# Kernel optimization log

Measured on AMD Instinct MI355X. Metric: run time of the kernel, lower is better.

The kernel has to match this reference:

```python
import jax, jax.numpy as jnp
import numpy as np

NUM_USERS = 100000
NUM_ITEMS = 100000
EMBED_DIM = 64
BATCH = 4096
MAX_NEIGH = 50


def setup_inputs() -> dict:
    key = jax.random.key(0)
    ks = jax.random.split(key, 12)
    d = EMBED_DIM
    nodes = jax.random.randint(ks[0], (BATCH,), 0, NUM_USERS)
    neighbors = jax.random.randint(ks[1], (BATCH, MAX_NEIGH), 0, NUM_ITEMS)
    lengths = 1 + jax.random.randint(ks[2], (BATCH,), 0, MAX_NEIGH)  # ragged sizes in [1, MAX_NEIGH]
    u_table = jax.random.normal(ks[3], (NUM_USERS, d), dtype=jnp.float32) * 0.1
    i_table = jax.random.normal(ks[4], (NUM_ITEMS, d), dtype=jnp.float32) * 0.1
    # GraphRec-style attention MLP: Linear(2d,d) -> relu -> Linear(d,d) -> relu -> Linear(d,1) -> softmax
    W1 = jax.random.normal(ks[5], (2 * d, d), dtype=jnp.float32) * (1.0 / np.sqrt(2 * d))
    b1 = jnp.zeros((d,), dtype=jnp.float32)
    W2 = jax.random.normal(ks[6], (d, d), dtype=jnp.float32) * (1.0 / np.sqrt(d))
    b2 = jnp.zeros((d,), dtype=jnp.float32)
    W3 = jax.random.normal(ks[7], (d, 1), dtype=jnp.float32) * (1.0 / np.sqrt(d))
    b3 = jnp.zeros((1,), dtype=jnp.float32)
    return {"u_table": u_table, "i_table": i_table, "W1": W1, "b1": b1,
            "W2": W2, "b2": b2, "W3": W3, "b3": b3,
            "nodes": nodes, "neighbors": neighbors, "lengths": lengths}


def reference(u_table, i_table, W1, b1, W2, b2, W3, b3, nodes, neighbors, lengths):
    # is_user=True: gather item features for neighbors, user feature for the node itself.
    neighs = i_table[neighbors]            # [B, L, d]
    node = u_table[nodes]                  # [B, d]
    B, L, d = neighs.shape
    x = jnp.concatenate([neighs, jnp.broadcast_to(node[:, None, :], (B, L, d))], axis=-1)  # [B, L, 2d]
    h = jax.nn.relu(x @ W1 + b1)           # [B, L, d]
    h = jax.nn.relu(h @ W2 + b2)           # [B, L, d]
    logits = (h @ W3 + b3)[..., 0]         # [B, L]
    mask = jnp.arange(L)[None, :] < lengths[:, None]  # ragged neighbor mask
    logits = jnp.where(mask, logits, -jnp.inf)
    att = jax.nn.softmax(logits, axis=1)   # softmax over each node's neighbors (dim=0 per-node in torch)
    # embedding = (neighs^T att)^T  ==  sum_l att[b,l] * neighs[b,l,:]
    return jnp.einsum("bl,bld->bd", att, neighs)  # [B, d]
```

## Files before the change

### kernel.cpp

```cpp
#include <hip/hip_runtime.h>
#include <math.h>

#define LMAX  50
#define NWAVE 2048

typedef short bf16x8 __attribute__((ext_vector_type(8)));
typedef float f32x4  __attribute__((ext_vector_type(4)));
union bfu { bf16x8 v; unsigned u[4]; };

__device__ __forceinline__ unsigned cvt_pk(float lo, float hi) {
    unsigned r;
    asm("v_cvt_pk_bf16_f32 %0, %1, %2" : "=v"(r) : "v"(lo), "v"(hi));
    return r;
}
__device__ __forceinline__ bf16x8 cvt8f(float4 a, float4 b) {
    bfu r;
    r.u[0] = cvt_pk(a.x, a.y); r.u[1] = cvt_pk(a.z, a.w);
    r.u[2] = cvt_pk(b.x, b.y); r.u[3] = cvt_pk(b.z, b.w);
    return r.v;
}

__device__ __forceinline__ void process_elem(
    const float* __restrict__ i_table, float* __restrict__ out,
    int b, int len, const int (&idx)[6],
    bf16x8 axu0, bf16x8 axu1,
    const bf16x8 (&w1f)[4][4], const bf16x8 (&w2f)[2][4],
    const float (&b1v)[4], const float (&b2v)[4], const float (&w3v)[4],
    unsigned short* __restrict__ hw, float* __restrict__ Lsw,
    int l15, int g)
{
    const int g8    = g * 8;
    const int ntile = (len + 15) >> 4;

    float4 LA[2][4];
    #define ISSUE_T(t) if ((t) < ntile) { \
        const float* xp = i_table + (size_t)idx[t] * 64 + g8; \
        LA[(t) & 1][0] = *(const float4*)(xp); \
        LA[(t) & 1][1] = *(const float4*)(xp + 4); \
        LA[(t) & 1][2] = *(const float4*)(xp + 32); \
        LA[(t) & 1][3] = *(const float4*)(xp + 36); \
    }
    ISSUE_T(0)
    ISSUE_T(1)

    f32x4 hn[4];
    #pragma unroll
    for (int nt = 0; nt < 4; ++nt)
        hn[nt] = (f32x4){b1v[nt], b1v[nt], b1v[nt], b1v[nt]};
    #pragma unroll
    for (int nt = 0; nt < 4; ++nt)
        hn[nt] = __builtin_amdgcn_mfma_f32_16x16x32_bf16(axu0, w1f[2][nt], hn[nt], 0, 0, 0);
    #pragma unroll
    for (int nt = 0; nt < 4; ++nt)
        hn[nt] = __builtin_amdgcn_mfma_f32_16x16x32_bf16(axu1, w1f[3][nt], hn[nt], 0, 0, 0);

    float m = -INFINITY, ssum = 0.f;
    float accW[16];
    #pragma unroll
    for (int i = 0; i < 16; ++i) accW[i] = 0.f;

    #pragma unroll
    for (int t = 0; t < 4; ++t) {
        if (t < ntile) {
            bf16x8 a0 = cvt8f(LA[t & 1][0], LA[t & 1][1]);
            bf16x8 a1 = cvt8f(LA[t & 1][2], LA[t & 1][3]);
            if (t + 2 < 4) ISSUE_T(t + 2)

            f32x4 acc[4];
            #pragma unroll
            for (int nt = 0; nt < 4; ++nt) acc[nt] = hn[nt];
            #pragma unroll
            for (int nt = 0; nt < 4; ++nt)
                acc[nt] = __builtin_amdgcn_mfma_f32_16x16x32_bf16(a0, w1f[0][nt], acc[nt], 0, 0, 0);
            #pragma unroll
            for (int nt = 0; nt < 4; ++nt)
                acc[nt] = __builtin_amdgcn_mfma_f32_16x16x32_bf16(a1, w1f[1][nt], acc[nt], 0, 0, 0);

            #pragma unroll
            for (int nt = 0; nt < 4; ++nt) {
                unsigned p0 = cvt_pk(fmaxf(acc[nt][0], 0.f), fmaxf(acc[nt][1], 0.f));
                unsigned p1 = cvt_pk(fmaxf(acc[nt][2], 0.f), fmaxf(acc[nt][3], 0.f));
                hw[(g * 4 + 0) * 72 + nt * 16 + l15] = (unsigned short)p0;
                hw[(g * 4 + 1) * 72 + nt * 16 + l15] = (unsigned short)(p0 >> 16);
                hw[(g * 4 + 2) * 72 + nt * 16 + l15] = (unsigned short)p1;
                hw[(g * 4 + 3) * 72 + nt * 16 + l15] = (unsigned short)(p1 >> 16);
            }
            bf16x8 h0 = *(const bf16x8*)&hw[l15 * 72 + g8];
            bf16x8 h1 = *(const bf16x8*)&hw[l15 * 72 + 32 + g8];

            f32x4 c2[4];
            #pragma unroll
            for (int nt = 0; nt < 4; ++nt)
                c2[nt] = (f32x4){b2v[nt], b2v[nt], b2v[nt], b2v[nt]};
            #pragma unroll
            for (int nt = 0; nt < 4; ++nt)
                c2[nt] = __builtin_amdgcn_mfma_f32_16x16x32_bf16(h0, w2f[0][nt], c2[nt], 0, 0, 0);
            #pragma unroll
            for (int nt = 0; nt < 4; ++nt)
                c2[nt] = __builtin_amdgcn_mfma_f32_16x16x32_bf16(h1, w2f[1][nt], c2[nt], 0, 0, 0);

            float sv[4];
            #pragma unroll
            for (int reg = 0; reg < 4; ++reg) {
                float s = 0.f;
                #pragma unroll
                for (int nt = 0; nt < 4; ++nt)
                    s = fmaf(fmaxf(c2[nt][reg], 0.f), w3v[nt], s);
                s += __shfl_xor(s, 1); s += __shfl_xor(s, 2);
                s += __shfl_xor(s, 4); s += __shfl_xor(s, 8);
                if (t * 16 + g * 4 + reg >= len) s = -INFINITY;
                sv[reg] = s;
            }

            float tm = fmaxf(fmaxf(sv[0], sv[1]), fmaxf(sv[2], sv[3]));
            tm = fmaxf(tm, __shfl_xor(tm, 16));
            tm = fmaxf(tm, __shfl_xor(tm, 32));
            if (tm > m) {
                const float nm = tm;
                const float sc = __expf(m - nm);
                ssum *= sc;
                #pragma unroll
                for (int i = 0; i < 16; ++i) accW[i] *= sc;
                m = nm;
            }
            float e0 = __expf(sv[0] - m), e1 = __expf(sv[1] - m);
            float e2 = __expf(sv[2] - m), e3 = __expf(sv[3] - m);
            float es = (e0 + e1) + (e2 + e3);
            es += __shfl_xor(es, 16);
            es += __shfl_xor(es, 32);
            ssum += es;

            if (l15 == 0) *(float4*)&Lsw[g * 4] = make_float4(e0, e1, e2, e3);
            const float er = Lsw[l15];

            #pragma unroll
            for (int i = 0; i < 8; ++i) {
                union { unsigned u; float f; } lo, hi2;
                lo.u  = ((unsigned)(unsigned short)a0[i]) << 16;
                hi2.u = ((unsigned)(unsigned short)a1[i]) << 16;
                accW[i]     = fmaf(er, lo.f,  accW[i]);
                accW[8 + i] = fmaf(er, hi2.f, accW[8 + i]);
            }
        }
    }
    #undef ISSUE_T

    #pragma unroll
    for (int i = 0; i < 16; ++i) {
        accW[i] += __shfl_xor(accW[i], 1);
        accW[i] += __shfl_xor(accW[i], 2);
        accW[i] += __shfl_xor(accW[i], 4);
        accW[i] += __shfl_xor(accW[i], 8);
    }
    const float inv = 1.f / ssum;
    if (l15 == 0) {
        float4 o0 = make_float4(accW[0] * inv,  accW[1] * inv,  accW[2] * inv,  accW[3] * inv);
        float4 o1 = make_float4(accW[4] * inv,  accW[5] * inv,  accW[6] * inv,  accW[7] * inv);
        float4 o2 = make_float4(accW[8] * inv,  accW[9] * inv,  accW[10] * inv, accW[11] * inv);
        float4 o3 = make_float4(accW[12] * inv, accW[13] * inv, accW[14] * inv, accW[15] * inv);
        *(float4*)(out + b * 64 +      g8)     = o0;
        *(float4*)(out + b * 64 +      g8 + 4) = o1;
        *(float4*)(out + b * 64 + 32 + g8)     = o2;
        *(float4*)(out + b * 64 + 32 + g8 + 4) = o3;
    }
}

__global__ __launch_bounds__(256, 2) void graphrec_k(
    const float* __restrict__ u_table, const float* __restrict__ i_table,
    const float* __restrict__ W1, const float* __restrict__ b1,
    const float* __restrict__ W2, const float* __restrict__ b2,
    const float* __restrict__ W3, const float* __restrict__ b3,
    const int* __restrict__ nodes, const int* __restrict__ neighbors,
    const int* __restrict__ lengths, float* __restrict__ out)
{
    __shared__ __attribute__((aligned(16))) short WL[24][64][8];
    __shared__ __attribute__((aligned(16))) unsigned short Hs[4][16 * 72];
    __shared__ float Ls[4][16];

    const int tid  = threadIdx.x;
    const int w    = tid >> 6, lane = tid & 63;
    const int l15  = lane & 15, g = lane >> 4, g8 = g * 8;

    for (int f = w; f < 24; f += 4) {
        const float* Ws = (f < 16) ? W1 : W2;
        const int    fi = (f < 16) ? f : f - 16;
        const int    ks = fi >> 2, nt = fi & 3;
        const float* p  = Ws + (ks * 32 + g8) * 64 + nt * 16 + l15;
        bfu r;
        r.u[0] = cvt_pk(p[0 * 64], p[1 * 64]);
        r.u[1] = cvt_pk(p[2 * 64], p[3 * 64]);
        r.u[2] = cvt_pk(p[4 * 64], p[5 * 64]);
        r.u[3] = cvt_pk(p[6 * 64], p[7 * 64]);
        *(bf16x8*)&WL[f][lane][0] = r.v;
    }
    __syncthreads();

    bf16x8 w1f[4][4], w2f[2][4];
    #pragma unroll
    for (int ks = 0; ks < 4; ++ks)
        #pragma unroll
        for (int nt = 0; nt < 4; ++nt)
            w1f[ks][nt] = *(const bf16x8*)&WL[ks * 4 + nt][lane][0];
    #pragma unroll
    for (int ks = 0; ks < 2; ++ks)
        #pragma unroll
        for (int nt = 0; nt < 4; ++nt)
            w2f[ks][nt] = *(const bf16x8*)&WL[16 + ks * 4 + nt][lane][0];

    float b1v[4], b2v[4], w3v[4];
    #pragma unroll
    for (int nt = 0; nt < 4; ++nt) {
        b1v[nt] = b1[nt * 16 + l15];
        b2v[nt] = b2[nt * 16 + l15];
        w3v[nt] = W3[nt * 16 + l15];
    }

    const int wid = blockIdx.x * 4 + w;
    const int b0  = wid, b1e = wid + NWAVE;

    const int len0 = lengths[b0], len1 = lengths[b1e];
    const int nd0  = nodes[b0],   nd1  = nodes[b1e];

    int idx0[6] = {0, 0, 0, 0, 0, 0}, idx1[6] = {0, 0, 0, 0, 0, 0};
    const int nt0 = (len0 + 15) >> 4, nt1 = (len1 + 15) >> 4;
    #pragma unroll
    for (int t = 0; t < 4; ++t) {
        int r = t * 16 + l15; if (r >= len0) r = len0 - 1;
        if (t < nt0) idx0[t] = neighbors[b0 * LMAX + r];
    }
    #pragma unroll
    for (int t = 0; t < 4; ++t) {
        int r = t * 16 + l15; if (r >= len1) r = len1 - 1;
        if (t < nt1) idx1[t] = neighbors[b1e * LMAX + r];
    }

    const float* up0 = u_table + (size_t)nd0 * 64 + g8;
    const float* up1 = u_table + (size_t)nd1 * 64 + g8;
    float4 U00 = *(const float4*)(up0);
    float4 U01 = *(const float4*)(up0 + 4);
    float4 U02 = *(const float4*)(up0 + 32);
    float4 U03 = *(const float4*)(up0 + 36);
    float4 U10 = *(const float4*)(up1);
    float4 U11 = *(const float4*)(up1 + 4);
    float4 U12 = *(const float4*)(up1 + 32);
    float4 U13 = *(const float4*)(up1 + 36);

    process_elem(i_table, out, b0, len0, idx0,
                 cvt8f(U00, U01), cvt8f(U02, U03),
                 w1f, w2f, b1v, b2v, w3v, &Hs[w][0], &Ls[w][0], l15, g);

    process_elem(i_table, out, b1e, len1, idx1,
                 cvt8f(U10, U11), cvt8f(U12, U13),
                 w1f, w2f, b1v, b2v, w3v, &Hs[w][0], &Ls[w][0], l15, g);
}

extern "C" void kernel_launch(void* const* d_in, const int* in_sizes, int n_in,
                              void* d_out, int out_size, void* d_ws, size_t ws_size,
                              hipStream_t stream) {
    const float* u_table   = (const float*)d_in[0];
    const float* i_table   = (const float*)d_in[1];
    const float* W1        = (const float*)d_in[2];
    const float* b1        = (const float*)d_in[3];
    const float* W2        = (const float*)d_in[4];
    const float* b2        = (const float*)d_in[5];
    const float* W3        = (const float*)d_in[6];
    const float* b3        = (const float*)d_in[7];
    const int*   nodes     = (const int*)d_in[8];
    const int*   neighbors = (const int*)d_in[9];
    const int*   lengths   = (const int*)d_in[10];
    float* out = (float*)d_out;

    graphrec_k<<<dim3(NWAVE / 4), dim3(256), 0, stream>>>(
        u_table, i_table, W1, b1, W2, b2, W3, b3, nodes, neighbors, lengths, out);
}
```

Measured before the change: 22.83 us.

## Process one batch element per wave and issue all gathers before weight staging

Each wave now handles a single batch element instead of two, which doubles the grid to 1024 blocks. All neighbor-row gathers (up to four tiles) and the user-row load are issued up front, before the weights are converted into shared memory, so gather latency overlaps with the weight setup and the barrier. The node-side W1 fragments are read directly from LDS rather than kept in registers, which frees registers for the larger in-flight load buffer. In exchange, every block repeats the weight conversion for half as many elements, and the indices past the row length fall back to lane 0's index via readlane.

```diff
diff --git a/kernel.cpp b/kernel.cpp
--- a/kernel.cpp
+++ b/kernel.cpp
@@ -1,8 +1,8 @@
 #include <hip/hip_runtime.h>
 #include <math.h>
 
-#define LMAX  50
-#define NWAVE 2048
+#define LMAX 50
+#define NB   4096
 
 typedef short bf16x8 __attribute__((ext_vector_type(8)));
 typedef float f32x4  __attribute__((ext_vector_type(4)));
@@ -19,150 +19,9 @@
     r.u[2] = cvt_pk(b.x, b.y); r.u[3] = cvt_pk(b.z, b.w);
     return r.v;
 }
-
-__device__ __forceinline__ void process_elem(
-    const float* __restrict__ i_table, float* __restrict__ out,
-    int b, int len, const int (&idx)[6],
-    bf16x8 axu0, bf16x8 axu1,
-    const bf16x8 (&w1f)[4][4], const bf16x8 (&w2f)[2][4],
-    const float (&b1v)[4], const float (&b2v)[4], const float (&w3v)[4],
-    unsigned short* __restrict__ hw, float* __restrict__ Lsw,
-    int l15, int g)
-{
-    const int g8    = g * 8;
-    const int ntile = (len + 15) >> 4;
-
-    float4 LA[2][4];
-    #define ISSUE_T(t) if ((t) < ntile) { \
-        const float* xp = i_table + (size_t)idx[t] * 64 + g8; \
-        LA[(t) & 1][0] = *(const float4*)(xp); \
-        LA[(t) & 1][1] = *(const float4*)(xp + 4); \
-        LA[(t) & 1][2] = *(const float4*)(xp + 32); \
-        LA[(t) & 1][3] = *(const float4*)(xp + 36); \
-    }
-    ISSUE_T(0)
-    ISSUE_T(1)
-
-    f32x4 hn[4];
-    #pragma unroll
-    for (int nt = 0; nt < 4; ++nt)
-        hn[nt] = (f32x4){b1v[nt], b1v[nt], b1v[nt], b1v[nt]};
-    #pragma unroll
-    for (int nt = 0; nt < 4; ++nt)
-        hn[nt] = __builtin_amdgcn_mfma_f32_16x16x32_bf16(axu0, w1f[2][nt], hn[nt], 0, 0, 0);
-    #pragma unroll
-    for (int nt = 0; nt < 4; ++nt)
-        hn[nt] = __builtin_amdgcn_mfma_f32_16x16x32_bf16(axu1, w1f[3][nt], hn[nt], 0, 0, 0);
-
-    float m = -INFINITY, ssum = 0.f;
-    float accW[16];
-    #pragma unroll
-    for (int i = 0; i < 16; ++i) accW[i] = 0.f;
-
-    #pragma unroll
-    for (int t = 0; t < 4; ++t) {
-        if (t < ntile) {
-            bf16x8 a0 = cvt8f(LA[t & 1][0], LA[t & 1][1]);
-            bf16x8 a1 = cvt8f(LA[t & 1][2], LA[t & 1][3]);
-            if (t + 2 < 4) ISSUE_T(t + 2)
-
-            f32x4 acc[4];
-            #pragma unroll
-            for (int nt = 0; nt < 4; ++nt) acc[nt] = hn[nt];
-            #pragma unroll
-            for (int nt = 0; nt < 4; ++nt)
-                acc[nt] = __builtin_amdgcn_mfma_f32_16x16x32_bf16(a0, w1f[0][nt], acc[nt], 0, 0, 0);
-            #pragma unroll
-            for (int nt = 0; nt < 4; ++nt)
-                acc[nt] = __builtin_amdgcn_mfma_f32_16x16x32_bf16(a1, w1f[1][nt], acc[nt], 0, 0, 0);
-
-            #pragma unroll
-            for (int nt = 0; nt < 4; ++nt) {
-                unsigned p0 = cvt_pk(fmaxf(acc[nt][0], 0.f), fmaxf(acc[nt][1], 0.f));
-                unsigned p1 = cvt_pk(fmaxf(acc[nt][2], 0.f), fmaxf(acc[nt][3], 0.f));
-                hw[(g * 4 + 0) * 72 + nt * 16 + l15] = (unsigned short)p0;
-                hw[(g * 4 + 1) * 72 + nt * 16 + l15] = (unsigned short)(p0 >> 16);
-                hw[(g * 4 + 2) * 72 + nt * 16 + l15] = (unsigned short)p1;
-                hw[(g * 4 + 3) * 72 + nt * 16 + l15] = (unsigned short)(p1 >> 16);
-            }
-            bf16x8 h0 = *(const bf16x8*)&hw[l15 * 72 + g8];
-            bf16x8 h1 = *(const bf16x8*)&hw[l15 * 72 + 32 + g8];
-
-            f32x4 c2[4];
-            #pragma unroll
-            for (int nt = 0; nt < 4; ++nt)
-                c2[nt] = (f32x4){b2v[nt], b2v[nt], b2v[nt], b2v[nt]};
-            #pragma unroll
-            for (int nt = 0; nt < 4; ++nt)
-                c2[nt] = __builtin_amdgcn_mfma_f32_16x16x32_bf16(h0, w2f[0][nt], c2[nt], 0, 0, 0);
-            #pragma unroll
-            for (int nt = 0; nt < 4; ++nt)
-                c2[nt] = __builtin_amdgcn_mfma_f32_16x16x32_bf16(h1, w2f[1][nt], c2[nt], 0, 0, 0);
-
-            float sv[4];
-            #pragma unroll
-            for (int reg = 0; reg < 4; ++reg) {
-                float s = 0.f;
-                #pragma unroll
-                for (int nt = 0; nt < 4; ++nt)
-                    s = fmaf(fmaxf(c2[nt][reg], 0.f), w3v[nt], s);
-                s += __shfl_xor(s, 1); s += __shfl_xor(s, 2);
-                s += __shfl_xor(s, 4); s += __shfl_xor(s, 8);
-                if (t * 16 + g * 4 + reg >= len) s = -INFINITY;
-                sv[reg] = s;
-            }
-
-            float tm = fmaxf(fmaxf(sv[0], sv[1]), fmaxf(sv[2], sv[3]));
-            tm = fmaxf(tm, __shfl_xor(tm, 16));
-            tm = fmaxf(tm, __shfl_xor(tm, 32));
-            if (tm > m) {
-                const float nm = tm;
-                const float sc = __expf(m - nm);
-                ssum *= sc;
-                #pragma unroll
-                for (int i = 0; i < 16; ++i) accW[i] *= sc;
-                m = nm;
-            }
-            float e0 = __expf(sv[0] - m), e1 = __expf(sv[1] - m);
-            float e2 = __expf(sv[2] - m), e3 = __expf(sv[3] - m);
-            float es = (e0 + e1) + (e2 + e3);
-            es += __shfl_xor(es, 16);
-            es += __shfl_xor(es, 32);
-            ssum += es;
-
-            if (l15 == 0) *(float4*)&Lsw[g * 4] = make_float4(e0, e1, e2, e3);
-            const float er = Lsw[l15];
-
-            #pragma unroll
-            for (int i = 0; i < 8; ++i) {
-                union { unsigned u; float f; } lo, hi2;
-                lo.u  = ((unsigned)(unsigned short)a0[i]) << 16;
-                hi2.u = ((unsigned)(unsigned short)a1[i]) << 16;
-                accW[i]     = fmaf(er, lo.f,  accW[i]);
-                accW[8 + i] = fmaf(er, hi2.f, accW[8 + i]);
-            }
-        }
-    }
-    #undef ISSUE_T
-
-    #pragma unroll
-    for (int i = 0; i < 16; ++i) {
-        accW[i] += __shfl_xor(accW[i], 1);
-        accW[i] += __shfl_xor(accW[i], 2);
-        accW[i] += __shfl_xor(accW[i], 4);
-        accW[i] += __shfl_xor(accW[i], 8);
-    }
-    const float inv = 1.f / ssum;
-    if (l15 == 0) {
-        float4 o0 = make_float4(accW[0] * inv,  accW[1] * inv,  accW[2] * inv,  accW[3] * inv);
-        float4 o1 = make_float4(accW[4] * inv,  accW[5] * inv,  accW[6] * inv,  accW[7] * inv);
-        float4 o2 = make_float4(accW[8] * inv,  accW[9] * inv,  accW[10] * inv, accW[11] * inv);
-        float4 o3 = make_float4(accW[12] * inv, accW[13] * inv, accW[14] * inv, accW[15] * inv);
-        *(float4*)(out + b * 64 +      g8)     = o0;
-        *(float4*)(out + b * 64 +      g8 + 4) = o1;
-        *(float4*)(out + b * 64 + 32 + g8)     = o2;
-        *(float4*)(out + b * 64 + 32 + g8 + 4) = o3;
-    }
+__device__ __forceinline__ float bf2f(short s) {
+    union { unsigned u; float f; } v; v.u = ((unsigned)(unsigned short)s) << 16;
+    return v.f;
 }
 
 __global__ __launch_bounds__(256, 2) void graphrec_k(
@@ -177,35 +36,19 @@
     __shared__ __attribute__((aligned(16))) unsigned short Hs[4][16 * 72];
     __shared__ float Ls[4][16];
 
-    const int tid  = threadIdx.x;
-    const int w    = tid >> 6, lane = tid & 63;
-    const int l15  = lane & 15, g = lane >> 4, g8 = g * 8;
-
-    for (int f = w; f < 24; f += 4) {
-        const float* Ws = (f < 16) ? W1 : W2;
-        const int    fi = (f < 16) ? f : f - 16;
-        const int    ks = fi >> 2, nt = fi & 3;
-        const float* p  = Ws + (ks * 32 + g8) * 64 + nt * 16 + l15;
-        bfu r;
-        r.u[0] = cvt_pk(p[0 * 64], p[1 * 64]);
-        r.u[1] = cvt_pk(p[2 * 64], p[3 * 64]);
-        r.u[2] = cvt_pk(p[4 * 64], p[5 * 64]);
-        r.u[3] = cvt_pk(p[6 * 64], p[7 * 64]);
-        *(bf16x8*)&WL[f][lane][0] = r.v;
-    }
-    __syncthreads();
-
-    bf16x8 w1f[4][4], w2f[2][4];
-    #pragma unroll
-    for (int ks = 0; ks < 4; ++ks)
-        #pragma unroll
-        for (int nt = 0; nt < 4; ++nt)
-            w1f[ks][nt] = *(const bf16x8*)&WL[ks * 4 + nt][lane][0];
-    #pragma unroll
-    for (int ks = 0; ks < 2; ++ks)
-        #pragma unroll
-        for (int nt = 0; nt < 4; ++nt)
-            w2f[ks][nt] = *(const bf16x8*)&WL[16 + ks * 4 + nt][lane][0];
+    const int tid = threadIdx.x;
+    const int w = tid >> 6, lane = tid & 63;
+    const int l15 = lane & 15, g = lane >> 4, g8 = g * 8;
+
+    const int b   = blockIdx.x * 4 + w;
+    const int len = lengths[b];
+    const int nd  = nodes[b];
+
+    int idxs[4];
+    idxs[0] = neighbors[b * LMAX + l15];
+    idxs[1] = neighbors[b * LMAX + 16 + l15];
+    idxs[2] = neighbors[b * LMAX + 32 + l15];
+    idxs[3] = neighbors[b * LMAX + min(48 + l15, LMAX - 1)];
 
     float b1v[4], b2v[4], w3v[4];
     #pragma unroll
@@ -215,43 +58,167 @@
         w3v[nt] = W3[nt * 16 + l15];
     }
 
-    const int wid = blockIdx.x * 4 + w;
-    const int b0  = wid, b1e = wid + NWAVE;
-
-    const int len0 = lengths[b0], len1 = lengths[b1e];
-    const int nd0  = nodes[b0],   nd1  = nodes[b1e];
-
-    int idx0[6] = {0, 0, 0, 0, 0, 0}, idx1[6] = {0, 0, 0, 0, 0, 0};
-    const int nt0 = (len0 + 15) >> 4, nt1 = (len1 + 15) >> 4;
+    const float* up = u_table + (size_t)nd * 64 + g8;
+    const float4 un0 = *(const float4*)(up);
+    const float4 un1 = *(const float4*)(up + 4);
+    const float4 un2 = *(const float4*)(up + 32);
+    const float4 un3 = *(const float4*)(up + 36);
+
+    const int ntl = (len + 15) >> 4;
+    float4 LA[4][4];
     #pragma unroll
     for (int t = 0; t < 4; ++t) {
-        int r = t * 16 + l15; if (r >= len0) r = len0 - 1;
-        if (t < nt0) idx0[t] = neighbors[b0 * LMAX + r];
-    }
+        if (t < ntl) {
+            const int fbv = __builtin_amdgcn_readlane(idxs[t], 0);
+            const int rr  = t * 16 + l15;
+            const int a   = (rr < len) ? idxs[t] : fbv;
+            const float* xp = i_table + (size_t)a * 64 + g8;
+            LA[t][0] = *(const float4*)(xp);
+            LA[t][1] = *(const float4*)(xp + 4);
+            LA[t][2] = *(const float4*)(xp + 32);
+            LA[t][3] = *(const float4*)(xp + 36);
+        }
+    }
+
+    for (int f = w; f < 24; f += 4) {
+        const float* Ws = (f < 16) ? W1 : W2;
+        const int fi = (f < 16) ? f : f - 16;
+        const int ks = fi >> 2, nt = fi & 3;
+        const float* p = Ws + (ks * 32 + g8) * 64 + nt * 16 + l15;
+        bfu r;
+        r.u[0] = cvt_pk(p[0],   p[64]);
+        r.u[1] = cvt_pk(p[128], p[192]);
+        r.u[2] = cvt_pk(p[256], p[320]);
+        r.u[3] = cvt_pk(p[384], p[448]);
+        *(bf16x8*)&WL[f][lane][0] = r.v;
+    }
+    __syncthreads();
+
+    bf16x8 w1f[2][4], w2f[2][4];
+    #pragma unroll
+    for (int ks = 0; ks < 2; ++ks)
+        #pragma unroll
+        for (int nt = 0; nt < 4; ++nt) {
+            w1f[ks][nt] = *(const bf16x8*)&WL[ks * 4 + nt][lane][0];
+            w2f[ks][nt] = *(const bf16x8*)&WL[16 + ks * 4 + nt][lane][0];
+        }
+
+    bf16x8 axu0 = cvt8f(un0, un1), axu1 = cvt8f(un2, un3);
+    f32x4 hn[4];
+    #pragma unroll
+    for (int nt = 0; nt < 4; ++nt) {
+        f32x4 c = { b1v[nt], b1v[nt], b1v[nt], b1v[nt] };
+        c = __builtin_amdgcn_mfma_f32_16x16x32_bf16(axu0, *(const bf16x8*)&WL[8  + nt][lane][0], c, 0, 0, 0);
+        c = __builtin_amdgcn_mfma_f32_16x16x32_bf16(axu1, *(const bf16x8*)&WL[12 + nt][lane][0], c, 0, 0, 0);
+        hn[nt] = c;
+    }
+
+    float m = -INFINITY, ssum = 0.f;
+    float accW[16];
+    #pragma unroll
+    for (int i = 0; i < 16; ++i) accW[i] = 0.f;
+
+    unsigned short* hw  = &Hs[w][0];
+    float*          Lsw = &Ls[w][0];
+
     #pragma unroll
     for (int t = 0; t < 4; ++t) {
-        int r = t * 16 + l15; if (r >= len1) r = len1 - 1;
-        if (t < nt1) idx1[t] = neighbors[b1e * LMAX + r];
-    }
-
-    const float* up0 = u_table + (size_t)nd0 * 64 + g8;
-    const float* up1 = u_table + (size_t)nd1 * 64 + g8;
-    float4 U00 = *(const float4*)(up0);
-    float4 U01 = *(const float4*)(up0 + 4);
-    float4 U02 = *(const float4*)(up0 + 32);
-    float4 U03 = *(const float4*)(up0 + 36);
-    float4 U10 = *(const float4*)(up1);
-    float4 U11 = *(const float4*)(up1 + 4);
-    float4 U12 = *(const float4*)(up1 + 32);
-    float4 U13 = *(const float4*)(up1 + 36);
-
-    process_elem(i_table, out, b0, len0, idx0,
-                 cvt8f(U00, U01), cvt8f(U02, U03),
-                 w1f, w2f, b1v, b2v, w3v, &Hs[w][0], &Ls[w][0], l15, g);
-
-    process_elem(i_table, out, b1e, len1, idx1,
-                 cvt8f(U10, U11), cvt8f(U12, U13),
-                 w1f, w2f, b1v, b2v, w3v, &Hs[w][0], &Ls[w][0], l15, g);
+        if (t < ntl) {
+            bf16x8 a0 = cvt8f(LA[t][0], LA[t][1]);
+            bf16x8 a1 = cvt8f(LA[t][2], LA[t][3]);
+
+            f32x4 acc[4];
+            #pragma unroll
+            for (int nt = 0; nt < 4; ++nt) acc[nt] = hn[nt];
+            #pragma unroll
+            for (int nt = 0; nt < 4; ++nt)
+                acc[nt] = __builtin_amdgcn_mfma_f32_16x16x32_bf16(a0, w1f[0][nt], acc[nt], 0, 0, 0);
+            #pragma unroll
+            for (int nt = 0; nt < 4; ++nt)
+                acc[nt] = __builtin_amdgcn_mfma_f32_16x16x32_bf16(a1, w1f[1][nt], acc[nt], 0, 0, 0);
+
+            #pragma unroll
+            for (int nt = 0; nt < 4; ++nt) {
+                unsigned p0 = cvt_pk(fmaxf(acc[nt][0], 0.f), fmaxf(acc[nt][1], 0.f));
+                unsigned p1 = cvt_pk(fmaxf(acc[nt][2], 0.f), fmaxf(acc[nt][3], 0.f));
+                hw[(g * 4 + 0) * 72 + nt * 16 + l15] = (unsigned short)p0;
+                hw[(g * 4 + 1) * 72 + nt * 16 + l15] = (unsigned short)(p0 >> 16);
+                hw[(g * 4 + 2) * 72 + nt * 16 + l15] = (unsigned short)p1;
+                hw[(g * 4 + 3) * 72 + nt * 16 + l15] = (unsigned short)(p1 >> 16);
+            }
+            bf16x8 h0 = *(const bf16x8*)&hw[l15 * 72 + g8];
+            bf16x8 h1 = *(const bf16x8*)&hw[l15 * 72 + 32 + g8];
+
+            f32x4 c2[4];
+            #pragma unroll
+            for (int nt = 0; nt < 4; ++nt)
+                c2[nt] = (f32x4){b2v[nt], b2v[nt], b2v[nt], b2v[nt]};
+            #pragma unroll
+            for (int nt = 0; nt < 4; ++nt)
+                c2[nt] = __builtin_amdgcn_mfma_f32_16x16x32_bf16(h0, w2f[0][nt], c2[nt], 0, 0, 0);
+            #pragma unroll
+            for (int nt = 0; nt < 4; ++nt)
+                c2[nt] = __builtin_amdgcn_mfma_f32_16x16x32_bf16(h1, w2f[1][nt], c2[nt], 0, 0, 0);
+
+            float sv[4];
+            #pragma unroll
+            for (int reg = 0; reg < 4; ++reg) {
+                float s = 0.f;
+                #pragma unroll
+                for (int nt = 0; nt < 4; ++nt)
+                    s = fmaf(fmaxf(c2[nt][reg], 0.f), w3v[nt], s);
+                s += __shfl_xor(s, 1); s += __shfl_xor(s, 2);
+                s += __shfl_xor(s, 4); s += __shfl_xor(s, 8);
+                if (t * 16 + g * 4 + reg >= len) s = -INFINITY;
+                sv[reg] = s;
+            }
+
+            float tm = fmaxf(fmaxf(sv[0], sv[1]), fmaxf(sv[2], sv[3]));
+            tm = fmaxf(tm, __shfl_xor(tm, 16));
+            tm = fmaxf(tm, __shfl_xor(tm, 32));
+            if (tm > m) {
+                const float sc = __expf(m - tm);
+                ssum *= sc;
+                #pragma unroll
+                for (int i = 0; i < 16; ++i) accW[i] *= sc;
+                m = tm;
+            }
+            float e0 = __expf(sv[0] - m), e1 = __expf(sv[1] - m);
+            float e2 = __expf(sv[2] - m), e3 = __expf(sv[3] - m);
+            float es = (e0 + e1) + (e2 + e3);
+            es += __shfl_xor(es, 16);
+            es += __shfl_xor(es, 32);
+            ssum += es;
+
+            if (l15 == 0) *(float4*)&Lsw[g * 4] = make_float4(e0, e1, e2, e3);
+            const float er = Lsw[l15];
+
+            #pragma unroll
+            for (int i = 0; i < 8; ++i) {
+                accW[i]     = fmaf(er, bf2f(a0[i]), accW[i]);
+                accW[8 + i] = fmaf(er, bf2f(a1[i]), accW[8 + i]);
+            }
+        }
+    }
+
+    #pragma unroll
+    for (int i = 0; i < 16; ++i) {
+        accW[i] += __shfl_xor(accW[i], 1);
+        accW[i] += __shfl_xor(accW[i], 2);
+        accW[i] += __shfl_xor(accW[i], 4);
+        accW[i] += __shfl_xor(accW[i], 8);
+    }
+    const float inv = 1.f / ssum;
+    if (l15 == 0) {
+        float4 o0 = make_float4(accW[0]  * inv, accW[1]  * inv, accW[2]  * inv, accW[3]  * inv);
+        float4 o1 = make_float4(accW[4]  * inv, accW[5]  * inv, accW[6]  * inv, accW[7]  * inv);
+        float4 o2 = make_float4(accW[8]  * inv, accW[9]  * inv, accW[10] * inv, accW[11] * inv);
+        float4 o3 = make_float4(accW[12] * inv, accW[13] * inv, accW[14] * inv, accW[15] * inv);
+        *(float4*)(out + b * 64 +      g8)     = o0;
+        *(float4*)(out + b * 64 +      g8 + 4) = o1;
+        *(float4*)(out + b * 64 + 32 + g8)     = o2;
+        *(float4*)(out + b * 64 + 32 + g8 + 4) = o3;
+    }
 }
 
 extern "C" void kernel_launch(void* const* d_in, const int* in_sizes, int n_in,
@@ -270,6 +237,6 @@
     const int*   lengths   = (const int*)d_in[10];
     float* out = (float*)d_out;
 
-    graphrec_k<<<dim3(NWAVE / 4), dim3(256), 0, stream>>>(
+    graphrec_k<<<dim3(NB / 4), dim3(256), 0, stream>>>(
         u_table, i_table, W1, b1, W2, b2, W3, b3, nodes, neighbors, lengths, out);
 }
```

After: 25.11 us. +10.0%, slower.
